# Kernel tuning notes

Measured on AMD Instinct MI355X. Metric: run time of the kernel, lower is better.

Reference implementation:

```python
import jax, jax.numpy as jnp
import numpy as np

B, L, C, H = 1, 2048, 2048, 16
D = C // H
EPS = 1e-6
W0 = 30.0  # SIREN frequency

def rmsnorm(x, w, eps=EPS):
    return x * jax.lax.rsqrt(jnp.mean(x * x, axis=-1, keepdims=True) + eps) * w

def depth_rope(x, depth, base=10000.0):
    # same rotation for all positions, angle set by scalar layer depth
    d = x.shape[-1]
    half = d // 2
    freqs = 1.0 / base ** (jnp.arange(half, dtype=x.dtype) / half)
    ang = depth * freqs
    cos, sin = jnp.cos(ang), jnp.sin(ang)
    x1, x2 = x[..., :half], x[..., half:2 * half]
    return jnp.concatenate([x1 * cos - x2 * sin, x1 * sin + x2 * cos], axis=-1)

def setup_inputs() -> dict:
    key = jax.random.key(0)
    ks = jax.random.split(key, 13)
    s = 1.0 / np.sqrt(C)
    inp = {
        'x':  jax.random.normal(ks[0], (B, L, C), jnp.float32),
        'h0': jax.random.normal(ks[1], (B, L, C), jnp.float32),
        'h1': jax.random.normal(ks[2], (B, L, C), jnp.float32),
        'h2': jax.random.normal(ks[3], (B, L, C), jnp.float32),
        'Wq': jax.random.normal(ks[4], (C, C), jnp.float32) * s,
        'Wk': jax.random.normal(ks[5], (C, C), jnp.float32) * s,
        'Wv': jax.random.normal(ks[6], (C, C), jnp.float32) * s,
        'Wo': jax.random.normal(ks[7], (C, C), jnp.float32) * s,
        'qn_w': jnp.ones((D,), jnp.float32),
        'kn_w': jnp.ones((D,), jnp.float32),
        'on_w': jnp.ones((C,), jnp.float32),
        'sw1': jax.random.normal(ks[8], (1, C), jnp.float32),
        'sb1': jax.random.normal(ks[9], (C,), jnp.float32) * 0.01,
        'sw2': jax.random.normal(ks[10], (C, C), jnp.float32) * s,
        'sb2': jnp.zeros((C,), jnp.float32),
    }
    return inp

def reference(x, h0, h1, h2, Wq, Wk, Wv, Wo, qn_w, kn_w, on_w, sw1, sb1, sw2, sb2):
    history = [h0, h1, h2]
    q_src = history[-1]                      # [B,L,C]
    q_depth = len(history) - 1
    # Q path: proj -> per-head RMSNorm -> depth RoPE
    q = jnp.einsum('blc,oc->blo', q_src, Wq).reshape(B, L, H, D)
    q = depth_rope(rmsnorm(q, qn_w), q_depth)
    # K/V path over prior history entries (each with its own depth)
    k_parts, v_parts = [], []
    for depth_idx, kv in enumerate(history[:-1]):
        k_i = jnp.einsum('blc,oc->blo', kv, Wk).reshape(B, L, H, D)
        v_i = jnp.einsum('blc,oc->blo', kv, Wv).reshape(B, L, H, D)
        k_parts.append(depth_rope(rmsnorm(k_i, kn_w), depth_idx))
        v_parts.append(v_i)
    k = jnp.concatenate(k_parts, axis=1)     # [B,Lkv,H,D]
    v = jnp.concatenate(v_parts, axis=1)
    # full SDPA, default scale D^-0.5
    scores = jnp.einsum('bqhd,bkhd->bhqk', q, k) * (D ** -0.5)
    attn = jax.nn.softmax(scores, axis=-1)
    out = jnp.einsum('bhqk,bkhd->bqhd', attn, v).reshape(B, L, C)
    out = jnp.einsum('blc,oc->blo', out, Wo)
    # SIREN upsample to (L,): target length == L -> identity interpolation
    # plus sine-activated coordinate MLP (implicit positional field)
    coords = jnp.linspace(-1.0, 1.0, L, dtype=x.dtype)[:, None]   # [L,1]
    pos = jnp.sin(W0 * (coords @ sw1 + sb1)) @ sw2 + sb2           # [L,C]
    out = out + pos[None]
    return x + rmsnorm(out, on_w)
```

## Files before the change

kernel.cpp:

```cpp
#include <hip/hip_runtime.h>
#include <hip/hip_fp16.h>

#define LQ 2048
#define CDIM 2048
#define NHEAD 16
#define HDIM 128
#define LKEY 4096

typedef _Float16 f16x8 __attribute__((ext_vector_type(8)));
typedef _Float16 f16x4 __attribute__((ext_vector_type(4)));
typedef float f32x4 __attribute__((ext_vector_type(4)));

#define GLOAD_LDS16(g, s) __builtin_amdgcn_global_load_lds( \
    (const __attribute__((address_space(1))) void*)(g),     \
    (__attribute__((address_space(3))) void*)(s), 16, 0, 0)

#define MFMA16(a, b, c) __builtin_amdgcn_mfma_f32_16x16x32_f16(a, b, c, 0, 0, 0)

__device__ __forceinline__ void storeC(float* p, float v) { *p = v; }
__device__ __forceinline__ void storeC(__half* p, float v) { *p = __float2half(v); }
__device__ __forceinline__ float toF(float v) { return v; }
__device__ __forceinline__ float toF(__half v) { return __half2float(v); }

template <typename OutT>
__device__ __forceinline__ void gemm_body(
    const __half* __restrict__ A, const __half* __restrict__ B,
    OutT* __restrict__ C, int lda, int ldb, int ldc, int K,
    int bmA, int bmC, int bn)
{
    __shared__ __align__(16) __half lA[128 * 64];
    __shared__ __align__(16) __half lB[128 * 64];
    const int tid  = threadIdx.x;
    const int lane = tid & 63;
    const int wave = tid >> 6;
    const int r = tid >> 3;
    const int g = tid & 7;
    const __half* gA = A + (long)(bmA * 128 + r) * lda + ((g ^ (r & 7)) << 3);
    const __half* gB = B + (long)(bn * 128 + r) * ldb + ((g ^ (r & 7)) << 3);
    __half* lAp = lA + tid * 8;
    __half* lBp = lB + tid * 8;
    const int wr = (wave & 1) << 6;
    const int wc = (wave >> 1) << 6;
    const int l15 = lane & 15, quad = lane >> 4;

    f32x4 acc[4][4] = {};

    for (int kt = 0; kt < K; kt += 64) {
#pragma unroll
        for (int i = 0; i < 4; ++i) {
            GLOAD_LDS16(gA + (long)i * 32 * lda, lAp + i * 2048);
            GLOAD_LDS16(gB + (long)i * 32 * ldb, lBp + i * 2048);
        }
        gA += 64; gB += 64;
        __syncthreads();
#pragma unroll
        for (int kk = 0; kk < 2; ++kk) {
            f16x8 af[4], bfr[4];
#pragma unroll
            for (int mi = 0; mi < 4; ++mi) {
                const int m = wr + mi * 16 + l15;
                const int kg = kk * 4 + quad;
                af[mi] = *(const f16x8*)&lA[m * 64 + ((kg ^ (m & 7)) << 3)];
            }
#pragma unroll
            for (int ni = 0; ni < 4; ++ni) {
                const int n = wc + ni * 16 + l15;
                const int kg = kk * 4 + quad;
                bfr[ni] = *(const f16x8*)&lB[n * 64 + ((kg ^ (n & 7)) << 3)];
            }
#pragma unroll
            for (int mi = 0; mi < 4; ++mi)
#pragma unroll
                for (int ni = 0; ni < 4; ++ni)
                    acc[mi][ni] = MFMA16(af[mi], bfr[ni], acc[mi][ni]);
        }
        __syncthreads();
    }
    const int row0 = bmC * 128 + wr + quad * 4;
    const int col0 = bn * 128 + wc + l15;
#pragma unroll
    for (int mi = 0; mi < 4; ++mi)
#pragma unroll
        for (int ni = 0; ni < 4; ++ni)
#pragma unroll
            for (int rx = 0; rx < 4; ++rx)
                storeC(&C[(long)(row0 + mi * 16 + rx) * ldc + col0 + ni * 16],
                       acc[mi][ni][rx]);
}

__global__ __launch_bounds__(256, 2) void gemm_qkv(
    const __half* __restrict__ A, const __half* __restrict__ Bq,
    const __half* __restrict__ Bkv, __half* __restrict__ Cq,
    __half* __restrict__ Ckv)
{
    const int lin = blockIdx.x;
    if (lin < 1024) {
        const int bm = lin & 31, bn = lin >> 5;
        gemm_body<__half>(A, Bkv, Ckv, 2048, 2048, 4096, 2048, bm + 16, bm, bn);
    } else {
        const int l2 = lin - 1024;
        const int bm = l2 & 15, bn = l2 >> 4;
        gemm_body<__half>(A, Bq, Cq, 2048, 2048, 2048, 2048, bm, bm, bn);
    }
}

__global__ __launch_bounds__(256, 2) void gemm_sk(
    const __half* __restrict__ A, const __half* __restrict__ B,
    float* __restrict__ C, int lda, int ldb, int ldc, int Khalf)
{
    const int z = blockIdx.z;
    gemm_body<float>(A + z * Khalf, B + z * Khalf, C + (long)z * LQ * CDIM,
                     lda, ldb, ldc, Khalf, blockIdx.x, blockIdx.x, blockIdx.y);
}

__global__ __launch_bounds__(256, 2) void attn_tile(
    const __half* __restrict__ Qf,
    const __half* __restrict__ Kf,
    const __half* __restrict__ Vt,
    float* __restrict__ Opart,
    float* __restrict__ lsum)
{
    __shared__ __align__(16) __half lK[64 * 128];
    __shared__ __align__(16) __half lV[128 * 64];
    __shared__ __align__(16) __half pL[4 * 2 * 16 * 76];

    const int tid  = threadIdx.x;
    const int lane = tid & 63;
    const int wave = tid >> 6;
    const int l15  = lane & 15;
    const int quad = lane >> 4;
    const int h  = blockIdx.y >> 1;
    const int kc = blockIdx.y & 1;
    const int q0 = blockIdx.x * 128 + wave * 32;

    f16x8 aq[2][4];
#pragma unroll
    for (int mt = 0; mt < 2; ++mt)
#pragma unroll
        for (int ks = 0; ks < 4; ++ks)
            aq[mt][ks] = *(const f16x8*)&Qf[(long)(q0 + mt * 16 + l15) * CDIM +
                                            h * HDIM + ks * 32 + quad * 8];

    const int rK = tid >> 4;
    const int gK = tid & 15;
    const __half* srcK = Kf + (long)(kc * 2048 + rK) * 4096 + h * HDIM +
                         ((gK ^ (rK & 15)) << 3);
    const int rV = tid >> 3;
    const int gV = tid & 7;
    const __half* srcV = Vt + (long)(h * HDIM + rV) * (long)LKEY + kc * 2048 +
                         ((gV ^ (rV & 7)) << 3);
    __half* dstK = lK + tid * 8;
    __half* dstV = lV + tid * 8;

    f32x4 accO[2][8] = {};
    f32x4 l_acc[2] = {};

    for (int st = 0; st < 32; ++st) {
#pragma unroll
        for (int i = 0; i < 4; ++i) {
            GLOAD_LDS16(srcK + (long)(st * 64 + i * 16) * 4096, dstK + i * 2048);
            GLOAD_LDS16(srcV + (long)i * 32 * LKEY + st * 64, dstV + i * 2048);
        }
        __syncthreads();
        f32x4 s[2][4];
#pragma unroll
        for (int mt = 0; mt < 2; ++mt)
#pragma unroll
            for (int nt = 0; nt < 4; ++nt)
                s[mt][nt] = (f32x4){-10.f, -10.f, -10.f, -10.f};
#pragma unroll
        for (int nt = 0; nt < 4; ++nt) {
            const int n = nt * 16 + l15;
#pragma unroll
            for (int ks = 0; ks < 4; ++ks) {
                const f16x8 kf = *(const f16x8*)
                    &lK[n * 128 + (((ks * 4 + quad) ^ (n & 15)) << 3)];
                s[0][nt] = MFMA16(aq[0][ks], kf, s[0][nt]);
                s[1][nt] = MFMA16(aq[1][ks], kf, s[1][nt]);
            }
        }
#pragma unroll
        for (int mt = 0; mt < 2; ++mt)
#pragma unroll
            for (int nt = 0; nt < 4; ++nt)
#pragma unroll
                for (int r2 = 0; r2 < 4; ++r2) {
                    const float p = __builtin_amdgcn_exp2f(s[mt][nt][r2]);
                    l_acc[mt][r2] += p;
                    pL[((wave * 2 + mt) * 16 + quad * 4 + r2) * 76 +
                       nt * 16 + l15] = __float2half(p);
                }
        f16x8 ap[2][2];
#pragma unroll
        for (int mt = 0; mt < 2; ++mt) {
            ap[mt][0] = *(const f16x8*)&pL[((wave * 2 + mt) * 16 + l15) * 76 + quad * 8];
            ap[mt][1] = *(const f16x8*)&pL[((wave * 2 + mt) * 16 + l15) * 76 + 32 + quad * 8];
        }
#pragma unroll
        for (int nt2 = 0; nt2 < 8; ++nt2) {
            const int n2 = nt2 * 16 + l15;
            const f16x8 v0 = *(const f16x8*)&lV[n2 * 64 + ((quad ^ (n2 & 7)) << 3)];
            const f16x8 v1 = *(const f16x8*)&lV[n2 * 64 + (((4 + quad) ^ (n2 & 7)) << 3)];
            accO[0][nt2] = MFMA16(ap[0][0], v0, accO[0][nt2]);
            accO[0][nt2] = MFMA16(ap[0][1], v1, accO[0][nt2]);
            accO[1][nt2] = MFMA16(ap[1][0], v0, accO[1][nt2]);
            accO[1][nt2] = MFMA16(ap[1][1], v1, accO[1][nt2]);
        }
        __syncthreads();
    }

#pragma unroll
    for (int mt = 0; mt < 2; ++mt)
#pragma unroll
        for (int r2 = 0; r2 < 4; ++r2) {
            float v = l_acc[mt][r2];
            v += __shfl_xor(v, 1);
            v += __shfl_xor(v, 2);
            v += __shfl_xor(v, 4);
            v += __shfl_xor(v, 8);
            if (l15 == 0)
                atomicAdd(&lsum[h * LQ + q0 + mt * 16 + quad * 4 + r2], v);
        }
    float* Cp = Opart + (long)kc * LQ * CDIM + h * HDIM;
#pragma unroll
    for (int mt = 0; mt < 2; ++mt)
#pragma unroll
        for (int nt2 = 0; nt2 < 8; ++nt2)
#pragma unroll
            for (int rx = 0; rx < 4; ++rx)
                Cp[(long)(q0 + mt * 16 + quad * 4 + rx) * CDIM + nt2 * 16 + l15] =
                    accO[mt][nt2][rx];
}

__global__ __launch_bounds__(256) void merge_o(
    const float* __restrict__ Op, const float* __restrict__ lsum,
    __half* __restrict__ a2)
{
    const int row = blockIdx.x;
    const int c0  = threadIdx.x * 8;
    const float inv = 1.0f / lsum[(c0 >> 7) * LQ + row];
    const float* p0 = Op + (long)row * CDIM + c0;
    const float* p1 = p0 + (long)LQ * CDIM;
    union { f16x8 v; _Float16 e[8]; } o;
#pragma unroll
    for (int j = 0; j < 8; ++j)
        o.e[j] = (_Float16)((p0[j] + p1[j]) * inv);
    *(f16x8*)&a2[(long)row * 4096 + c0] = o.v;
}

__global__ __launch_bounds__(256) void norm_rope(
    __half* __restrict__ X, const float* __restrict__ w,
    int stride, int nrows, int kmode, float oscale)
{
    const int gid  = blockIdx.x * 4 + (threadIdx.x >> 6);
    const int lane = threadIdx.x & 63;
    const int row  = gid >> 4;
    const int h    = gid & 15;
    if (row >= nrows) return;
    __half* p = X + (long)row * stride + h * HDIM;
    float x1 = __half2float(p[lane]);
    float x2 = __half2float(p[lane + 64]);
    float ss = x1 * x1 + x2 * x2;
#pragma unroll
    for (int off = 1; off < 64; off <<= 1) ss += __shfl_xor(ss, off);
    const float rn = rsqrtf(ss * (1.0f / 128.0f) + 1e-6f);
    x1 *= rn * w[lane];
    x2 *= rn * w[lane + 64];
    const int depth = kmode ? (row < LQ ? 0 : 1) : 2;
    const float freq = exp2f(-(float)lane * 0.20762050593045702f);
    const float ang = (float)depth * freq;
    float sn, cs;
    __sincosf(ang, &sn, &cs);
    p[lane]      = __float2half((x1 * cs - x2 * sn) * oscale);
    p[lane + 64] = __float2half((x1 * sn + x2 * cs) * oscale);
}

__global__ __launch_bounds__(256) void cast_all(
    const float* __restrict__ h2, const float* __restrict__ h0,
    const float* __restrict__ h1, const float* __restrict__ Wq,
    const float* __restrict__ Wk, const float* __restrict__ Wv,
    __half* __restrict__ xq, __half* __restrict__ xkv,
    __half* __restrict__ wqh, __half* __restrict__ wkv)
{
    const long i = ((long)blockIdx.x * 256 + threadIdx.x) << 2;
    const int chunk = (int)(i >> 22);
    const long off = i & 4194303;
    const float* s; __half* d;
    switch (chunk) {
        case 0:  s = h2; d = xq;            break;
        case 1:  s = h0; d = xkv;           break;
        case 2:  s = h1; d = xkv + 4194304; break;
        case 3:  s = Wq; d = wqh;           break;
        case 4:  s = Wk; d = wkv;           break;
        default: s = Wv; d = wkv + 4194304; break;
    }
    const float4 v = *(const float4*)&s[off];
    f16x4 o;
    o[0] = (_Float16)v.x; o[1] = (_Float16)v.y;
    o[2] = (_Float16)v.z; o[3] = (_Float16)v.w;
    *(f16x4*)&d[off] = o;
}

__global__ void cast_wo(const float* __restrict__ in, __half* __restrict__ out) {
    const int idx = blockIdx.x * 256 + threadIdx.x;
    const int o = idx >> 11, c = idx & 2047;
    out[((long)o << 12) + c] = __float2half(in[idx]);
}

template <typename InT>
__global__ __launch_bounds__(256) void transpose_h(
    const InT* __restrict__ in, long inStride, long inOff,
    __half* __restrict__ out, long outStride, long outOff)
{
    __shared__ float t[64][65];
    const long r0 = (long)blockIdx.x * 64;
    const long c0 = (long)blockIdx.y * 64;
    const int tj = threadIdx.x & 63;
    const int ti = threadIdx.x >> 6;
#pragma unroll
    for (int it = 0; it < 16; ++it) {
        const int i = it * 4 + ti;
        t[i][tj] = toF(in[(r0 + i) * inStride + inOff + c0 + tj]);
    }
    __syncthreads();
#pragma unroll
    for (int it = 0; it < 16; ++it) {
        const int i = it * 4 + ti;
        out[(c0 + i) * outStride + outOff + r0 + tj] = __float2half(t[tj][i]);
    }
}

__global__ __launch_bounds__(256) void sin_feat(
    const float* __restrict__ sw1, const float* __restrict__ sb1,
    __half* __restrict__ a2)
{
    const int idx = (blockIdx.x * 256 + threadIdx.x) << 2;
    const int l = idx >> 11, c = idx & 2047;
    const float coord = -1.0f + (2.0f / 2047.0f) * (float)l;
    const float4 w = *(const float4*)&sw1[c];
    const float4 b = *(const float4*)&sb1[c];
    f16x4 o;
    o[0] = (_Float16)__sinf(30.0f * (coord * w.x + b.x));
    o[1] = (_Float16)__sinf(30.0f * (coord * w.y + b.y));
    o[2] = (_Float16)__sinf(30.0f * (coord * w.z + b.z));
    o[3] = (_Float16)__sinf(30.0f * (coord * w.w + b.w));
    *(f16x4*)&a2[((long)l << 12) + 2048 + c] = o;
}

__global__ __launch_bounds__(256) void final_norm(
    const float* __restrict__ out2, const float* __restrict__ x,
    const float* __restrict__ sb2, const float* __restrict__ on_w,
    float* __restrict__ y)
{
    const int row = blockIdx.x;
    const float* o0 = out2 + (long)row * CDIM;
    const float* o1 = o0 + (long)LQ * CDIM;
    float v[8];
    float ss = 0.f;
#pragma unroll
    for (int i = 0; i < 8; ++i) {
        const int c = threadIdx.x + i * 256;
        const float t = o0[c] + o1[c] + sb2[c];
        v[i] = t;
        ss += t * t;
    }
#pragma unroll
    for (int off = 1; off < 64; off <<= 1) ss += __shfl_xor(ss, off);
    __shared__ float red[4];
    const int lane = threadIdx.x & 63, wv = threadIdx.x >> 6;
    if (lane == 0) red[wv] = ss;
    __syncthreads();
    const float tot = red[0] + red[1] + red[2] + red[3];
    const float rn = rsqrtf(tot * (1.0f / 2048.0f) + 1e-6f);
#pragma unroll
    for (int i = 0; i < 8; ++i) {
        const int c = threadIdx.x + i * 256;
        y[(long)row * CDIM + c] = x[(long)row * CDIM + c] + v[i] * rn * on_w[c];
    }
}

extern "C" void kernel_launch(void* const* d_in, const int* in_sizes, int n_in,
                              void* d_out, int out_size, void* d_ws, size_t ws_size,
                              hipStream_t stream) {
    const float* x    = (const float*)d_in[0];
    const float* h0   = (const float*)d_in[1];
    const float* h1   = (const float*)d_in[2];
    const float* h2   = (const float*)d_in[3];
    const float* Wq   = (const float*)d_in[4];
    const float* Wk   = (const float*)d_in[5];
    const float* Wv   = (const float*)d_in[6];
    const float* Wo   = (const float*)d_in[7];
    const float* qn_w = (const float*)d_in[8];
    const float* kn_w = (const float*)d_in[9];
    const float* on_w = (const float*)d_in[10];
    const float* sw1  = (const float*)d_in[11];
    const float* sb1  = (const float*)d_in[12];
    const float* sw2  = (const float*)d_in[13];
    const float* sb2  = (const float*)d_in[14];
    float* y = (float*)d_out;

    const size_t MB = 1ull << 20;
    char* w = (char*)d_ws;
    __half* xq  = (__half*)(w);
    __half* xkv = (__half*)(w + 8 * MB);
    __half* wqh = (__half*)(w + 24 * MB);
    __half* wkv = (__half*)(w + 32 * MB);
    __half* qf  = (__half*)(w + 48 * MB);
    __half* kvf = (__half*)(w + 56 * MB);
    __half* vT  = (__half*)(w + 88 * MB);
    __half* a2  = (__half*)(w + 104 * MB);
    __half* b2  = (__half*)(w + 120 * MB);
    float* Opart = (float*)(w);
    float* lsum  = (float*)(w + 32 * MB);
    float* out2  = (float*)(w + 56 * MB);
    (void)in_sizes; (void)n_in; (void)out_size; (void)ws_size;

    const int n4 = 2048 * 2048;
    cast_all<<<24576, 256, 0, stream>>>(h2, h0, h1, Wq, Wk, Wv, xq, xkv, wqh, wkv);
    cast_wo<<<n4 / 256, 256, 0, stream>>>(Wo, b2);
    transpose_h<float><<<dim3(32, 32), 256, 0, stream>>>(sw2, 2048, 0, b2, 4096, 2048);
    sin_feat<<<4096, 256, 0, stream>>>(sw1, sb1, a2);

    gemm_qkv<<<1280, 256, 0, stream>>>(xq, wqh, wkv, qf, kvf);

    norm_rope<<<8192, 256, 0, stream>>>(qf, qn_w, 2048, 2048, 0, 0.12751743f);
    norm_rope<<<16384, 256, 0, stream>>>(kvf, kn_w, 4096, 4096, 1, 1.0f);
    transpose_h<__half><<<dim3(64, 32), 256, 0, stream>>>(kvf, 4096, 2048, vT, 4096, 0);

    (void)hipMemsetAsync(lsum, 0, NHEAD * LQ * sizeof(float), stream);
    attn_tile<<<dim3(16, 32), 256, 0, stream>>>(qf, kvf, vT, Opart, lsum);
    merge_o<<<2048, 256, 0, stream>>>(Opart, lsum, a2);

    gemm_sk<<<dim3(16, 16, 2), 256, 0, stream>>>(a2, b2, out2, 4096, 4096, 2048, 2048);
    final_norm<<<2048, 256, 0, stream>>>(out2, x, sb2, on_w, y);
}
```

Measured before the change: 454.1 us.

## Fuse norm/RoPE and V transpose into QKV GEMM epilogue; 4-way split-K output GEMM

The per-head RMSNorm plus depth RoPE for Q and K, and the V transpose, move into the QKV GEMM epilogue. The tile is staged through shared memory, or V is written directly transposed, which drops three separate kernels and their round-trips through global memory. The final output GEMM's split-K goes from 2 to 4 to launch more blocks, and final_norm now sums four partials. In exchange, the epilogue adds shared memory and compute, the direct transposed V store is uncoalesced, and the extra partials add memory traffic.

```diff
diff --git a/kernel.cpp b/kernel.cpp
--- a/kernel.cpp
+++ b/kernel.cpp
@@ -22,14 +22,17 @@
 __device__ __forceinline__ float toF(float v) { return v; }
 __device__ __forceinline__ float toF(__half v) { return __half2float(v); }
 
-template <typename OutT>
+template <int MODE, typename OutT>
 __device__ __forceinline__ void gemm_body(
+    __half* smem,
     const __half* __restrict__ A, const __half* __restrict__ B,
     OutT* __restrict__ C, int lda, int ldb, int ldc, int K,
-    int bmA, int bmC, int bn)
-{
-    __shared__ __align__(16) __half lA[128 * 64];
-    __shared__ __align__(16) __half lB[128 * 64];
+    int bmA, int bmC, int bn,
+    const float* __restrict__ wgt, int kmode, float oscale,
+    __half* __restrict__ vTo)
+{
+    __half* lA = smem;
+    __half* lB = smem + 8192;
     const int tid  = threadIdx.x;
     const int lane = tid & 63;
     const int wave = tid >> 6;
@@ -76,41 +79,118 @@
         }
         __syncthreads();
     }
-    const int row0 = bmC * 128 + wr + quad * 4;
-    const int col0 = bn * 128 + wc + l15;
-#pragma unroll
-    for (int mi = 0; mi < 4; ++mi)
-#pragma unroll
-        for (int ni = 0; ni < 4; ++ni)
-#pragma unroll
-            for (int rx = 0; rx < 4; ++rx)
-                storeC(&C[(long)(row0 + mi * 16 + rx) * ldc + col0 + ni * 16],
-                       acc[mi][ni][rx]);
+
+    if constexpr (MODE == 0) {
+        const int row0 = bmC * 128 + wr + quad * 4;
+        const int col0 = bn * 128 + wc + l15;
+#pragma unroll
+        for (int mi = 0; mi < 4; ++mi)
+#pragma unroll
+            for (int ni = 0; ni < 4; ++ni)
+#pragma unroll
+                for (int rx = 0; rx < 4; ++rx)
+                    storeC(&C[(long)(row0 + mi * 16 + rx) * ldc + col0 + ni * 16],
+                           acc[mi][ni][rx]);
+    } else if constexpr (MODE == 2) {
+#pragma unroll
+        for (int mi = 0; mi < 4; ++mi)
+#pragma unroll
+            for (int ni = 0; ni < 4; ++ni)
+#pragma unroll
+                for (int rx = 0; rx < 4; ++rx) {
+                    const int  d   = (bn - 16) * 128 + wc + ni * 16 + l15;
+                    const long key = (long)bmC * 128 + wr + mi * 16 + quad * 4 + rx;
+                    vTo[(long)d * LKEY + key] = __float2half(acc[mi][ni][rx]);
+                }
+    } else {
+        __half* sT = smem;
+#pragma unroll
+        for (int mi = 0; mi < 4; ++mi)
+#pragma unroll
+            for (int ni = 0; ni < 4; ++ni)
+#pragma unroll
+                for (int rx = 0; rx < 4; ++rx)
+                    sT[(wr + mi * 16 + quad * 4 + rx) * 136 + wc + ni * 16 + l15] =
+                        (_Float16)acc[mi][ni][rx];
+        __syncthreads();
+        const int row = (wave << 5) + (lane >> 1);
+        const int c0  = (lane & 1) << 5;
+        const __half* rp = sT + row * 136;
+        f16x8 L[4], Hh[4];
+#pragma unroll
+        for (int j8 = 0; j8 < 4; ++j8) {
+            L[j8]  = *(const f16x8*)&rp[c0 + j8 * 8];
+            Hh[j8] = *(const f16x8*)&rp[c0 + 64 + j8 * 8];
+        }
+        float ss = 0.f;
+#pragma unroll
+        for (int j8 = 0; j8 < 4; ++j8)
+#pragma unroll
+            for (int e = 0; e < 8; ++e) {
+                const float a = (float)L[j8][e], b = (float)Hh[j8][e];
+                ss += a * a + b * b;
+            }
+        ss += __shfl_xor(ss, 1);
+        const float rn = rsqrtf(ss * (1.0f / 128.0f) + 1e-6f);
+        const long grow = (long)bmC * 128 + row;
+        const int depth = kmode ? (grow < 2048 ? 0 : 1) : 2;
+        union { f16x8 v; _Float16 e[8]; } o1[4], o2[4];
+#pragma unroll
+        for (int j8 = 0; j8 < 4; ++j8)
+#pragma unroll
+            for (int e = 0; e < 8; ++e) {
+                const int d = c0 + j8 * 8 + e;
+                const float x1 = (float)L[j8][e]  * rn * wgt[d];
+                const float x2 = (float)Hh[j8][e] * rn * wgt[d + 64];
+                const float ang = (float)depth *
+                    exp2f(-(float)d * 0.20762050593045702f);
+                float sn, cs;
+                __sincosf(ang, &sn, &cs);
+                o1[j8].e[e] = (_Float16)((x1 * cs - x2 * sn) * oscale);
+                o2[j8].e[e] = (_Float16)((x1 * sn + x2 * cs) * oscale);
+            }
+        __half* op = (__half*)C + grow * ldc + bn * 128;
+#pragma unroll
+        for (int j8 = 0; j8 < 4; ++j8) {
+            *(f16x8*)&op[c0 + j8 * 8]      = o1[j8].v;
+            *(f16x8*)&op[c0 + 64 + j8 * 8] = o2[j8].v;
+        }
+    }
 }
 
 __global__ __launch_bounds__(256, 2) void gemm_qkv(
     const __half* __restrict__ A, const __half* __restrict__ Bq,
     const __half* __restrict__ Bkv, __half* __restrict__ Cq,
-    __half* __restrict__ Ckv)
-{
+    __half* __restrict__ Ckv, __half* __restrict__ vT,
+    const float* __restrict__ qn_w, const float* __restrict__ kn_w)
+{
+    __shared__ __align__(16) __half smem[17408];
     const int lin = blockIdx.x;
     if (lin < 1024) {
         const int bm = lin & 31, bn = lin >> 5;
-        gemm_body<__half>(A, Bkv, Ckv, 2048, 2048, 4096, 2048, bm + 16, bm, bn);
+        if (bn < 16)
+            gemm_body<1, __half>(smem, A, Bkv, Ckv, 2048, 2048, 4096, 2048,
+                                 bm + 16, bm, bn, kn_w, 1, 1.0f, nullptr);
+        else
+            gemm_body<2, __half>(smem, A, Bkv, Ckv, 2048, 2048, 4096, 2048,
+                                 bm + 16, bm, bn, nullptr, 0, 1.0f, vT);
     } else {
         const int l2 = lin - 1024;
         const int bm = l2 & 15, bn = l2 >> 4;
-        gemm_body<__half>(A, Bq, Cq, 2048, 2048, 2048, 2048, bm, bm, bn);
+        gemm_body<1, __half>(smem, A, Bq, Cq, 2048, 2048, 2048, 2048,
+                             bm, bm, bn, qn_w, 0, 0.12751743f, nullptr);
     }
 }
 
 __global__ __launch_bounds__(256, 2) void gemm_sk(
     const __half* __restrict__ A, const __half* __restrict__ B,
-    float* __restrict__ C, int lda, int ldb, int ldc, int Khalf)
-{
+    float* __restrict__ C, int lda, int ldb, int ldc, int Kq)
+{
+    __shared__ __align__(16) __half smem[16384];
     const int z = blockIdx.z;
-    gemm_body<float>(A + z * Khalf, B + z * Khalf, C + (long)z * LQ * CDIM,
-                     lda, ldb, ldc, Khalf, blockIdx.x, blockIdx.x, blockIdx.y);
+    gemm_body<0, float>(smem, A + z * Kq, B + z * Kq, C + (long)z * LQ * CDIM,
+                        lda, ldb, ldc, Kq, blockIdx.x, blockIdx.x, blockIdx.y,
+                        nullptr, 0, 1.0f, nullptr);
 }
 
 __global__ __launch_bounds__(256, 2) void attn_tile(
@@ -246,33 +326,6 @@
     for (int j = 0; j < 8; ++j)
         o.e[j] = (_Float16)((p0[j] + p1[j]) * inv);
     *(f16x8*)&a2[(long)row * 4096 + c0] = o.v;
-}
-
-__global__ __launch_bounds__(256) void norm_rope(
-    __half* __restrict__ X, const float* __restrict__ w,
-    int stride, int nrows, int kmode, float oscale)
-{
-    const int gid  = blockIdx.x * 4 + (threadIdx.x >> 6);
-    const int lane = threadIdx.x & 63;
-    const int row  = gid >> 4;
-    const int h    = gid & 15;
-    if (row >= nrows) return;
-    __half* p = X + (long)row * stride + h * HDIM;
-    float x1 = __half2float(p[lane]);
-    float x2 = __half2float(p[lane + 64]);
-    float ss = x1 * x1 + x2 * x2;
-#pragma unroll
-    for (int off = 1; off < 64; off <<= 1) ss += __shfl_xor(ss, off);
-    const float rn = rsqrtf(ss * (1.0f / 128.0f) + 1e-6f);
-    x1 *= rn * w[lane];
-    x2 *= rn * w[lane + 64];
-    const int depth = kmode ? (row < LQ ? 0 : 1) : 2;
-    const float freq = exp2f(-(float)lane * 0.20762050593045702f);
-    const float ang = (float)depth * freq;
-    float sn, cs;
-    __sincosf(ang, &sn, &cs);
-    p[lane]      = __float2half((x1 * cs - x2 * sn) * oscale);
-    p[lane + 64] = __float2half((x1 * sn + x2 * cs) * oscale);
 }
 
 __global__ __launch_bounds__(256) void cast_all(
@@ -354,13 +407,15 @@
 {
     const int row = blockIdx.x;
     const float* o0 = out2 + (long)row * CDIM;
-    const float* o1 = o0 + (long)LQ * CDIM;
+    const float* o1 = o0 + 1l * LQ * CDIM;
+    const float* o2 = o0 + 2l * LQ * CDIM;
+    const float* o3 = o0 + 3l * LQ * CDIM;
     float v[8];
     float ss = 0.f;
 #pragma unroll
     for (int i = 0; i < 8; ++i) {
         const int c = threadIdx.x + i * 256;
-        const float t = o0[c] + o1[c] + sb2[c];
+        const float t = o0[c] + o1[c] + o2[c] + o3[c] + sb2[c];
         v[i] = t;
         ss += t * t;
     }
@@ -412,7 +467,7 @@
     __half* b2  = (__half*)(w + 120 * MB);
     float* Opart = (float*)(w);
     float* lsum  = (float*)(w + 32 * MB);
-    float* out2  = (float*)(w + 56 * MB);
+    float* out2  = (float*)(w);
     (void)in_sizes; (void)n_in; (void)out_size; (void)ws_size;
 
     const int n4 = 2048 * 2048;
@@ -421,16 +476,12 @@
     transpose_h<float><<<dim3(32, 32), 256, 0, stream>>>(sw2, 2048, 0, b2, 4096, 2048);
     sin_feat<<<4096, 256, 0, stream>>>(sw1, sb1, a2);
 
-    gemm_qkv<<<1280, 256, 0, stream>>>(xq, wqh, wkv, qf, kvf);
-
-    norm_rope<<<8192, 256, 0, stream>>>(qf, qn_w, 2048, 2048, 0, 0.12751743f);
-    norm_rope<<<16384, 256, 0, stream>>>(kvf, kn_w, 4096, 4096, 1, 1.0f);
-    transpose_h<__half><<<dim3(64, 32), 256, 0, stream>>>(kvf, 4096, 2048, vT, 4096, 0);
+    gemm_qkv<<<1280, 256, 0, stream>>>(xq, wqh, wkv, qf, kvf, vT, qn_w, kn_w);
 
     (void)hipMemsetAsync(lsum, 0, NHEAD * LQ * sizeof(float), stream);
     attn_tile<<<dim3(16, 32), 256, 0, stream>>>(qf, kvf, vT, Opart, lsum);
     merge_o<<<2048, 256, 0, stream>>>(Opart, lsum, a2);
 
-    gemm_sk<<<dim3(16, 16, 2), 256, 0, stream>>>(a2, b2, out2, 4096, 4096, 2048, 2048);
+    gemm_sk<<<dim3(16, 16, 4), 256, 0, stream>>>(a2, b2, out2, 4096, 4096, 2048, 1024);
     final_norm<<<2048, 256, 0, stream>>>(out2, x, sb2, on_w, y);
 }
```

Result: no change. 457.4 us (+0.7%).
